# Optimization experiments

Hardware: AMD Instinct MI355X
Metric: run time of the kernel (lower is better)

## Reference

```python
import jax, jax.numpy as jnp
import numpy as np

N_NODES = 50000
N_EDGES = 600000
IN_FEATS = 128
N_HIDDEN = 128
N_CLASSES = 64


def setup_inputs() -> dict:
    key = jax.random.key(0)
    ks = jax.random.split(key, 10)
    x = jax.random.normal(ks[0], (N_NODES, IN_FEATS), dtype=jnp.float32)
    w = jax.random.uniform(ks[1], (N_EDGES,), dtype=jnp.float32)
    src = jax.random.randint(ks[2], (N_EDGES,), 0, N_NODES, dtype=jnp.int32)
    dst = jax.random.randint(ks[3], (N_EDGES,), 0, N_NODES, dtype=jnp.int32)
    W1 = jax.random.normal(ks[4], (IN_FEATS, N_HIDDEN), dtype=jnp.float32) * 0.05
    b1 = jnp.zeros((N_HIDDEN,), dtype=jnp.float32)
    W2 = jax.random.normal(ks[5], (N_HIDDEN, N_HIDDEN), dtype=jnp.float32) * 0.05
    b2 = jnp.zeros((N_HIDDEN,), dtype=jnp.float32)
    W3 = jax.random.normal(ks[6], (N_HIDDEN, N_CLASSES), dtype=jnp.float32) * 0.05
    b3 = jnp.zeros((N_CLASSES,), dtype=jnp.float32)
    return {"x": x, "w": w, "src": src, "dst": dst,
            "W1": W1, "b1": b1, "W2": W2, "b2": b2, "W3": W3, "b3": b3}


def _graph_conv(h, Wl, bl, w, src, dst, n_nodes):
    # dense linear transform
    h = h @ Wl + bl  # [N, d_out]
    # u_mul_e: gather source features, scale by edge weight
    m = h[src] * w[:, None]  # [E, d_out]
    # sum aggregation into destination nodes
    return jax.ops.segment_sum(m, dst, num_segments=n_nodes)  # [N, d_out]


def reference(x, w, src, dst, W1, b1, W2, b2, W3, b3):
    n = x.shape[0]
    h = jax.nn.relu(_graph_conv(x, W1, b1, w, src, dst, n))
    h = jax.nn.relu(_graph_conv(h, W2, b2, w, src, dst, n))
    return _graph_conv(h, W3, b3, w, src, dst, n)
```

## Files before the change

### kernel.cpp

```cpp
#include <hip/hip_runtime.h>


typedef __attribute__((ext_vector_type(8))) short short8;
typedef __attribute__((ext_vector_type(4))) float float4v;

constexpr int CAP  = 48;
constexpr int CPAD = 16;

__device__ inline unsigned bf16_rne(float f) {
    unsigned u = __float_as_uint(f);
    return (u + 0x7FFF + ((u >> 16) & 1)) >> 16;
}
__device__ inline float bf_lo(unsigned t) { return __uint_as_float(t << 16); }
__device__ inline float bf_hi(unsigned t) { return __uint_as_float(t & 0xFFFF0000u); }

__device__ inline void wprep_one(const float* __restrict__ Wm, int M, int tt,
                                 unsigned short* __restrict__ WfH,
                                 unsigned short* __restrict__ WfL) {
    const int FT = M / 16;
    int lane = tt & 63;
    int ft   = (tt >> 6) % FT;
    int ks   = tt / (64 * FT);
    int n     = ft * 16 + (lane & 15);
    int kbase = ks * 32 + (lane >> 4) * 8;
    #pragma unroll
    for (int j = 0; j < 8; j++) {
        float wv = Wm[(size_t)(kbase + j) * M + n];
        unsigned hb = bf16_rne(wv);
        float wh = __uint_as_float(hb << 16);
        unsigned lb = bf16_rne(wv - wh);
        WfH[(size_t)tt * 8 + j] = (unsigned short)hb;
        WfL[(size_t)tt * 8 + j] = (unsigned short)lb;
    }
}

__global__ void prep_kernel(const float* __restrict__ W1, const float* __restrict__ W2,
                            const float* __restrict__ W3,
                            unsigned short* WfH1, unsigned short* WfL1,
                            unsigned short* WfH2, unsigned short* WfL2,
                            unsigned short* WfH3, unsigned short* WfL3,
                            int* __restrict__ countsP, int N) {
    int t = blockIdx.x * blockDim.x + threadIdx.x;
    if (t < 2048)       wprep_one(W1, 128, t,        WfH1, WfL1);
    else if (t < 4096)  wprep_one(W2, 128, t - 2048, WfH2, WfL2);
    else if (t < 5120)  wprep_one(W3,  64, t - 4096, WfH3, WfL3);
    const int total = N * CPAD;
    for (int i = t; i < total; i += gridDim.x * blockDim.x) countsP[i] = 0;
}

__global__ void scatter_v5(const int* __restrict__ src, const int* __restrict__ dst,
                           const float* __restrict__ w, int* __restrict__ countsP,
                           int2* __restrict__ erec, int E) {
    int e = (blockIdx.x * blockDim.x + threadIdx.x) * 4;
    if (e + 3 < E) {
        int4   d4 = *(const int4*)(dst + e);
        int4   s4 = *(const int4*)(src + e);
        float4 w4 = *(const float4*)(w + e);
        int p0 = atomicAdd(&countsP[d4.x * CPAD], 1);
        int p1 = atomicAdd(&countsP[d4.y * CPAD], 1);
        int p2 = atomicAdd(&countsP[d4.z * CPAD], 1);
        int p3 = atomicAdd(&countsP[d4.w * CPAD], 1);
        if (p0 < CAP) erec[(size_t)d4.x * CAP + p0] = (int2){s4.x, __float_as_int(w4.x)};
        if (p1 < CAP) erec[(size_t)d4.y * CAP + p1] = (int2){s4.y, __float_as_int(w4.y)};
        if (p2 < CAP) erec[(size_t)d4.z * CAP + p2] = (int2){s4.z, __float_as_int(w4.z)};
        if (p3 < CAP) erec[(size_t)d4.w * CAP + p3] = (int2){s4.w, __float_as_int(w4.w)};
    } else {
        for (; e < E; e++) {
            int d = dst[e];
            int p = atomicAdd(&countsP[d * CPAD], 1);
            if (p < CAP) erec[(size_t)d * CAP + p] = (int2){src[e], __float_as_int(w[e])};
        }
    }
}

template <int M>
__global__ __launch_bounds__(256) void gemm_kernel(const float* __restrict__ H,
                                                   const unsigned short* __restrict__ WfH,
                                                   const unsigned short* __restrict__ WfL,
                                                   const float* __restrict__ bias,
                                                   unsigned short* __restrict__ T, int N) {
    const int K  = 128;
    const int KP = K + 4;
    const int FT = M / 16;
    __shared__ float Hs[64 * KP];

    const int node0 = blockIdx.x * 64;
    for (int i = threadIdx.x; i < 64 * (K / 4); i += 256) {
        int r = i / (K / 4), c = i % (K / 4);
        int node = node0 + r;
        float4 hv = {0, 0, 0, 0};
        if (node < N) hv = ((const float4*)(H + (size_t)node * K))[c];
        *(float4*)(Hs + r * KP + c * 4) = hv;
    }
    __syncthreads();

    const int wave = threadIdx.x >> 6;
    const int lane = threadIdx.x & 63;
    const int row  = lane & 15;
    const int ksub = (lane >> 4) * 8;
    const float* hrow = Hs + (wave * 16 + row) * KP;

    float4v acc[FT];
    #pragma unroll
    for (int ft = 0; ft < FT; ft++) acc[ft] = (float4v){0.f, 0.f, 0.f, 0.f};

    #pragma unroll
    for (int ks = 0; ks < 4; ks++) {
        const float* ap = hrow + ks * 32 + ksub;
        float4 a0 = *(const float4*)(ap);
        float4 a1 = *(const float4*)(ap + 4);
        float av[8] = {a0.x, a0.y, a0.z, a0.w, a1.x, a1.y, a1.z, a1.w};
        short8 ah, al;
        #pragma unroll
        for (int j = 0; j < 8; j++) {
            unsigned hb = bf16_rne(av[j]);
            float fh = __uint_as_float(hb << 16);
            ah[j] = (short)hb;
            al[j] = (short)bf16_rne(av[j] - fh);
        }
        #pragma unroll
        for (int ft = 0; ft < FT; ft++) {
            short8 bh = *(const short8*)(WfH + ((size_t)(ks * FT + ft) * 64 + lane) * 8);
            short8 bl = *(const short8*)(WfL + ((size_t)(ks * FT + ft) * 64 + lane) * 8);
            acc[ft] = __builtin_amdgcn_mfma_f32_16x16x32_bf16(ah, bh, acc[ft], 0, 0, 0);
            acc[ft] = __builtin_amdgcn_mfma_f32_16x16x32_bf16(al, bh, acc[ft], 0, 0, 0);
            acc[ft] = __builtin_amdgcn_mfma_f32_16x16x32_bf16(ah, bl, acc[ft], 0, 0, 0);
        }
    }

    const int col   = lane & 15;
    const int rbase = (lane >> 4) * 4;
    #pragma unroll
    for (int ft = 0; ft < FT; ft++) {
        int feat = ft * 16 + col;
        float bv = bias[feat];
        #pragma unroll
        for (int r = 0; r < 4; r++) {
            int node = node0 + wave * 16 + rbase + r;
            if (node < N)
                T[(size_t)node * M + feat] = (unsigned short)bf16_rne(acc[ft][r] + bv);
        }
    }
}

template <bool RELU>
__global__ void agg128_v4(const unsigned short* __restrict__ Tin,
                          const int* __restrict__ countsP,
                          const int2* __restrict__ erec,
                          float* __restrict__ OUT, int N) {
    const int wid  = threadIdx.x >> 6;
    const int lane = threadIdx.x & 63;
    const int v = blockIdx.x * 4 + wid;
    if (v >= N) return;
    const int c = min(countsP[v * CPAD], CAP);
    const int q  = lane >> 4;
    const int fo = (lane & 15) * 8;
    float a0 = 0, a1 = 0, a2 = 0, a3 = 0, a4 = 0, a5 = 0, a6 = 0, a7 = 0;
    if (c > 0) {
        const int2* eb = erec + (size_t)v * CAP;
        for (int i = 0; i < c; i += 16) {
            #pragma unroll
            for (int u = 0; u < 4; u++) {
                int idx = i + u * 4 + q;
                float wv = 0.f;
                int cl = idx < c ? idx : c - 1;
                int2 r = eb[cl];
                if (idx < c) wv = __int_as_float(r.y);
                uint4 t = *(const uint4*)(Tin + (size_t)r.x * 128 + fo);
                a0 = fmaf(wv, bf_lo(t.x), a0); a1 = fmaf(wv, bf_hi(t.x), a1);
                a2 = fmaf(wv, bf_lo(t.y), a2); a3 = fmaf(wv, bf_hi(t.y), a3);
                a4 = fmaf(wv, bf_lo(t.z), a4); a5 = fmaf(wv, bf_hi(t.z), a5);
                a6 = fmaf(wv, bf_lo(t.w), a6); a7 = fmaf(wv, bf_hi(t.w), a7);
            }
        }
        a0 += __shfl_xor(a0, 32); a1 += __shfl_xor(a1, 32);
        a2 += __shfl_xor(a2, 32); a3 += __shfl_xor(a3, 32);
        a4 += __shfl_xor(a4, 32); a5 += __shfl_xor(a5, 32);
        a6 += __shfl_xor(a6, 32); a7 += __shfl_xor(a7, 32);
        a0 += __shfl_xor(a0, 16); a1 += __shfl_xor(a1, 16);
        a2 += __shfl_xor(a2, 16); a3 += __shfl_xor(a3, 16);
        a4 += __shfl_xor(a4, 16); a5 += __shfl_xor(a5, 16);
        a6 += __shfl_xor(a6, 16); a7 += __shfl_xor(a7, 16);
    }
    if (lane < 16) {
        if (RELU) {
            a0 = fmaxf(a0, 0.f); a1 = fmaxf(a1, 0.f); a2 = fmaxf(a2, 0.f); a3 = fmaxf(a3, 0.f);
            a4 = fmaxf(a4, 0.f); a5 = fmaxf(a5, 0.f); a6 = fmaxf(a6, 0.f); a7 = fmaxf(a7, 0.f);
        }
        float4 o0 = {a0, a1, a2, a3};
        float4 o1 = {a4, a5, a6, a7};
        float* op = OUT + (size_t)v * 128 + fo;
        *(float4*)(op)     = o0;
        *(float4*)(op + 4) = o1;
    }
}

__global__ void agg_final_v4(const unsigned short* __restrict__ Tin,
                             const int* __restrict__ countsP,
                             const int2* __restrict__ erec,
                             float* __restrict__ OUT, int N) {
    const int wid  = threadIdx.x >> 6;
    const int lane = threadIdx.x & 63;
    const int v = blockIdx.x * 4 + wid;
    if (v >= N) return;
    const int c = min(countsP[v * CPAD], CAP);
    const int o8 = lane >> 3;
    const int fo = (lane & 7) * 8;
    float a0 = 0, a1 = 0, a2 = 0, a3 = 0, a4 = 0, a5 = 0, a6 = 0, a7 = 0;
    if (c > 0) {
        const int2* eb = erec + (size_t)v * CAP;
        for (int i = 0; i < c; i += 16) {
            #pragma unroll
            for (int u = 0; u < 2; u++) {
                int idx = i + u * 8 + o8;
                float wv = 0.f;
                int cl = idx < c ? idx : c - 1;
                int2 r = eb[cl];
                if (idx < c) wv = __int_as_float(r.y);
                uint4 t = *(const uint4*)(Tin + (size_t)r.x * 64 + fo);
                a0 = fmaf(wv, bf_lo(t.x), a0); a1 = fmaf(wv, bf_hi(t.x), a1);
                a2 = fmaf(wv, bf_lo(t.y), a2); a3 = fmaf(wv, bf_hi(t.y), a3);
                a4 = fmaf(wv, bf_lo(t.z), a4); a5 = fmaf(wv, bf_hi(t.z), a5);
                a6 = fmaf(wv, bf_lo(t.w), a6); a7 = fmaf(wv, bf_hi(t.w), a7);
            }
        }
        a0 += __shfl_xor(a0, 32); a1 += __shfl_xor(a1, 32);
        a2 += __shfl_xor(a2, 32); a3 += __shfl_xor(a3, 32);
        a4 += __shfl_xor(a4, 32); a5 += __shfl_xor(a5, 32);
        a6 += __shfl_xor(a6, 32); a7 += __shfl_xor(a7, 32);
        a0 += __shfl_xor(a0, 16); a1 += __shfl_xor(a1, 16);
        a2 += __shfl_xor(a2, 16); a3 += __shfl_xor(a3, 16);
        a4 += __shfl_xor(a4, 16); a5 += __shfl_xor(a5, 16);
        a6 += __shfl_xor(a6, 16); a7 += __shfl_xor(a7, 16);
        a0 += __shfl_xor(a0, 8);  a1 += __shfl_xor(a1, 8);
        a2 += __shfl_xor(a2, 8);  a3 += __shfl_xor(a3, 8);
        a4 += __shfl_xor(a4, 8);  a5 += __shfl_xor(a5, 8);
        a6 += __shfl_xor(a6, 8);  a7 += __shfl_xor(a7, 8);
    }
    if (lane < 8) {
        float4 o0 = {a0, a1, a2, a3};
        float4 o1 = {a4, a5, a6, a7};
        float* op = OUT + (size_t)v * 64 + fo;
        *(float4*)(op)     = o0;
        *(float4*)(op + 4) = o1;
    }
}

extern "C" void kernel_launch(void* const* d_in, const int* in_sizes, int n_in,
                              void* d_out, int out_size, void* d_ws, size_t ws_size,
                              hipStream_t stream) {
    const float* x   = (const float*)d_in[0];
    const float* w   = (const float*)d_in[1];
    const int*   src = (const int*)d_in[2];
    const int*   dst = (const int*)d_in[3];
    const float* W1  = (const float*)d_in[4];
    const float* b1  = (const float*)d_in[5];
    const float* W2  = (const float*)d_in[6];
    const float* b2  = (const float*)d_in[7];
    const float* W3  = (const float*)d_in[8];
    const float* b3  = (const float*)d_in[9];
    const int N = in_sizes[0] / 128;
    const int E = in_sizes[1];

    float* Hf            = (float*)d_ws;
    unsigned short* Tbf  = (unsigned short*)(Hf + (size_t)N * 128);
    int2* erec     = (int2*)(Tbf + (size_t)N * 128);
    int*  countsP  = (int*)(erec + (size_t)N * CAP);
    size_t off = (size_t)(countsP + (size_t)N * CPAD - (int*)d_ws);
    off = (off + 3) & ~(size_t)3;
    unsigned short* WfH1 = (unsigned short*)((int*)d_ws + off);
    unsigned short* WfL1 = WfH1 + 128 * 128;
    unsigned short* WfH2 = WfL1 + 128 * 128;
    unsigned short* WfL2 = WfH2 + 128 * 128;
    unsigned short* WfH3 = WfL2 + 128 * 128;
    unsigned short* WfL3 = WfH3 + 128 * 64;

    const int GB = (N + 63) / 64;
    const int AB = (N + 3) / 4;

    prep_kernel<<<96, 256, 0, stream>>>(W1, W2, W3, WfH1, WfL1, WfH2, WfL2,
                                        WfH3, WfL3, countsP, N);
    gemm_kernel<128><<<GB, 256, 0, stream>>>(x, WfH1, WfL1, b1, Tbf, N);
    scatter_v5<<<(E / 4 + 255) / 256, 256, 0, stream>>>(src, dst, w, countsP, erec, E);
    agg128_v4<true><<<AB, 256, 0, stream>>>(Tbf, countsP, erec, Hf, N);
    gemm_kernel<128><<<GB, 256, 0, stream>>>(Hf, WfH2, WfL2, b2, Tbf, N);
    agg128_v4<true><<<AB, 256, 0, stream>>>(Tbf, countsP, erec, Hf, N);
    gemm_kernel<64><<<GB, 256, 0, stream>>>(Hf, WfH3, WfL3, b3, Tbf, N);
    agg_final_v4<<<AB, 256, 0, stream>>>(Tbf, countsP, erec, (float*)d_out, N);
}
```

Baseline: 243.7 us.

## Fuse aggregation with following GEMM through shared memory

Replaces the aggregation kernel plus the separate dense GEMM with one kernel. Each 1024-thread block aggregates 16 nodes into shared memory, applies ReLU, then runs split-bf16 MFMA against the next layer's weights and writes bf16 output. This removes the fp32 hidden-feature round trip through global memory and two kernel launches. In exchange, large blocks must synchronise before the GEMM, and only FT of the 16 waves do GEMM work while the rest sit idle, which may lower occupancy.

```diff
diff --git a/kernel.cpp b/kernel.cpp
--- a/kernel.cpp
+++ b/kernel.cpp
@@ -143,55 +143,104 @@
     }
 }
 
-template <bool RELU>
-__global__ void agg128_v4(const unsigned short* __restrict__ Tin,
-                          const int* __restrict__ countsP,
-                          const int2* __restrict__ erec,
-                          float* __restrict__ OUT, int N) {
-    const int wid  = threadIdx.x >> 6;
+template <int MOUT>
+__global__ __launch_bounds__(1024) void fused_agg_gemm(
+    const unsigned short* __restrict__ Tin,
+    const int* __restrict__ countsP,
+    const int2* __restrict__ erec,
+    const unsigned short* __restrict__ WfH,
+    const unsigned short* __restrict__ WfL,
+    const float* __restrict__ bias,
+    unsigned short* __restrict__ Tout,
+    int N) {
+    const int KP = 132;
+    __shared__ float Hs[16 * KP];
+    const int wave = threadIdx.x >> 6;
     const int lane = threadIdx.x & 63;
-    const int v = blockIdx.x * 4 + wid;
-    if (v >= N) return;
-    const int c = min(countsP[v * CPAD], CAP);
-    const int q  = lane >> 4;
-    const int fo = (lane & 15) * 8;
-    float a0 = 0, a1 = 0, a2 = 0, a3 = 0, a4 = 0, a5 = 0, a6 = 0, a7 = 0;
-    if (c > 0) {
-        const int2* eb = erec + (size_t)v * CAP;
-        for (int i = 0; i < c; i += 16) {
-            #pragma unroll
-            for (int u = 0; u < 4; u++) {
-                int idx = i + u * 4 + q;
-                float wv = 0.f;
-                int cl = idx < c ? idx : c - 1;
-                int2 r = eb[cl];
-                if (idx < c) wv = __int_as_float(r.y);
-                uint4 t = *(const uint4*)(Tin + (size_t)r.x * 128 + fo);
-                a0 = fmaf(wv, bf_lo(t.x), a0); a1 = fmaf(wv, bf_hi(t.x), a1);
-                a2 = fmaf(wv, bf_lo(t.y), a2); a3 = fmaf(wv, bf_hi(t.y), a3);
-                a4 = fmaf(wv, bf_lo(t.z), a4); a5 = fmaf(wv, bf_hi(t.z), a5);
-                a6 = fmaf(wv, bf_lo(t.w), a6); a7 = fmaf(wv, bf_hi(t.w), a7);
+    const int v = blockIdx.x * 16 + wave;
+
+    {
+        const int q  = lane >> 4;
+        const int fo = (lane & 15) * 8;
+        float a0 = 0, a1 = 0, a2 = 0, a3 = 0, a4 = 0, a5 = 0, a6 = 0, a7 = 0;
+        if (v < N) {
+            const int c = min(countsP[v * CPAD], CAP);
+            if (c > 0) {
+                const int2* eb = erec + (size_t)v * CAP;
+                for (int i = 0; i < c; i += 16) {
+                    #pragma unroll
+                    for (int u = 0; u < 4; u++) {
+                        int idx = i + u * 4 + q;
+                        float wv = 0.f;
+                        int cl = idx < c ? idx : c - 1;
+                        int2 r = eb[cl];
+                        if (idx < c) wv = __int_as_float(r.y);
+                        uint4 t = *(const uint4*)(Tin + (size_t)r.x * 128 + fo);
+                        a0 = fmaf(wv, bf_lo(t.x), a0); a1 = fmaf(wv, bf_hi(t.x), a1);
+                        a2 = fmaf(wv, bf_lo(t.y), a2); a3 = fmaf(wv, bf_hi(t.y), a3);
+                        a4 = fmaf(wv, bf_lo(t.z), a4); a5 = fmaf(wv, bf_hi(t.z), a5);
+                        a6 = fmaf(wv, bf_lo(t.w), a6); a7 = fmaf(wv, bf_hi(t.w), a7);
+                    }
+                }
+                a0 += __shfl_xor(a0, 32); a1 += __shfl_xor(a1, 32);
+                a2 += __shfl_xor(a2, 32); a3 += __shfl_xor(a3, 32);
+                a4 += __shfl_xor(a4, 32); a5 += __shfl_xor(a5, 32);
+                a6 += __shfl_xor(a6, 32); a7 += __shfl_xor(a7, 32);
+                a0 += __shfl_xor(a0, 16); a1 += __shfl_xor(a1, 16);
+                a2 += __shfl_xor(a2, 16); a3 += __shfl_xor(a3, 16);
+                a4 += __shfl_xor(a4, 16); a5 += __shfl_xor(a5, 16);
+                a6 += __shfl_xor(a6, 16); a7 += __shfl_xor(a7, 16);
             }
         }
-        a0 += __shfl_xor(a0, 32); a1 += __shfl_xor(a1, 32);
-        a2 += __shfl_xor(a2, 32); a3 += __shfl_xor(a3, 32);
-        a4 += __shfl_xor(a4, 32); a5 += __shfl_xor(a5, 32);
-        a6 += __shfl_xor(a6, 32); a7 += __shfl_xor(a7, 32);
-        a0 += __shfl_xor(a0, 16); a1 += __shfl_xor(a1, 16);
-        a2 += __shfl_xor(a2, 16); a3 += __shfl_xor(a3, 16);
-        a4 += __shfl_xor(a4, 16); a5 += __shfl_xor(a5, 16);
-        a6 += __shfl_xor(a6, 16); a7 += __shfl_xor(a7, 16);
-    }
-    if (lane < 16) {
-        if (RELU) {
+        if (lane < 16) {
             a0 = fmaxf(a0, 0.f); a1 = fmaxf(a1, 0.f); a2 = fmaxf(a2, 0.f); a3 = fmaxf(a3, 0.f);
             a4 = fmaxf(a4, 0.f); a5 = fmaxf(a5, 0.f); a6 = fmaxf(a6, 0.f); a7 = fmaxf(a7, 0.f);
-        }
-        float4 o0 = {a0, a1, a2, a3};
-        float4 o1 = {a4, a5, a6, a7};
-        float* op = OUT + (size_t)v * 128 + fo;
-        *(float4*)(op)     = o0;
-        *(float4*)(op + 4) = o1;
+            float* hp = Hs + wave * KP + lane * 8;
+            float4 o0 = {a0, a1, a2, a3};
+            float4 o1 = {a4, a5, a6, a7};
+            *(float4*)(hp)     = o0;
+            *(float4*)(hp + 4) = o1;
+        }
+    }
+    __syncthreads();
+
+    const int FT = MOUT / 16;
+    if (wave < FT) {
+        const int ft   = wave;
+        const int row  = lane & 15;
+        const int ksub = (lane >> 4) * 8;
+        const float* hrow = Hs + row * KP;
+        float4v acc = (float4v){0.f, 0.f, 0.f, 0.f};
+        #pragma unroll
+        for (int ks = 0; ks < 4; ks++) {
+            const float* ap = hrow + ks * 32 + ksub;
+            float4 A0 = *(const float4*)(ap);
+            float4 A1 = *(const float4*)(ap + 4);
+            float av[8] = {A0.x, A0.y, A0.z, A0.w, A1.x, A1.y, A1.z, A1.w};
+            short8 ah, al;
+            #pragma unroll
+            for (int j = 0; j < 8; j++) {
+                unsigned hb = bf16_rne(av[j]);
+                float fh = __uint_as_float(hb << 16);
+                ah[j] = (short)hb;
+                al[j] = (short)bf16_rne(av[j] - fh);
+            }
+            short8 bh = *(const short8*)(WfH + ((size_t)(ks * FT + ft) * 64 + lane) * 8);
+            short8 bl = *(const short8*)(WfL + ((size_t)(ks * FT + ft) * 64 + lane) * 8);
+            acc = __builtin_amdgcn_mfma_f32_16x16x32_bf16(ah, bh, acc, 0, 0, 0);
+            acc = __builtin_amdgcn_mfma_f32_16x16x32_bf16(al, bh, acc, 0, 0, 0);
+            acc = __builtin_amdgcn_mfma_f32_16x16x32_bf16(ah, bl, acc, 0, 0, 0);
+        }
+        const int col   = lane & 15;
+        const int rbase = (lane >> 4) * 4;
+        int feat = ft * 16 + col;
+        float bv = bias[feat];
+        #pragma unroll
+        for (int r = 0; r < 4; r++) {
+            int node = blockIdx.x * 16 + rbase + r;
+            if (node < N)
+                Tout[(size_t)node * MOUT + feat] = (unsigned short)bf16_rne(acc[r] + bv);
+        }
     }
 }
 
@@ -262,9 +311,9 @@
     const int N = in_sizes[0] / 128;
     const int E = in_sizes[1];
 
-    float* Hf            = (float*)d_ws;
-    unsigned short* Tbf  = (unsigned short*)(Hf + (size_t)N * 128);
-    int2* erec     = (int2*)(Tbf + (size_t)N * 128);
+    unsigned short* TbfA = (unsigned short*)d_ws;
+    unsigned short* TbfB = TbfA + (size_t)N * 128;
+    int2* erec     = (int2*)(TbfB + (size_t)N * 128);
     int*  countsP  = (int*)(erec + (size_t)N * CAP);
     size_t off = (size_t)(countsP + (size_t)N * CPAD - (int*)d_ws);
     off = (off + 3) & ~(size_t)3;
@@ -276,15 +325,16 @@
     unsigned short* WfL3 = WfH3 + 128 * 64;
 
     const int GB = (N + 63) / 64;
+    const int FB = (N + 15) / 16;
     const int AB = (N + 3) / 4;
 
     prep_kernel<<<96, 256, 0, stream>>>(W1, W2, W3, WfH1, WfL1, WfH2, WfL2,
                                         WfH3, WfL3, countsP, N);
-    gemm_kernel<128><<<GB, 256, 0, stream>>>(x, WfH1, WfL1, b1, Tbf, N);
+    gemm_kernel<128><<<GB, 256, 0, stream>>>(x, WfH1, WfL1, b1, TbfA, N);
     scatter_v5<<<(E / 4 + 255) / 256, 256, 0, stream>>>(src, dst, w, countsP, erec, E);
-    agg128_v4<true><<<AB, 256, 0, stream>>>(Tbf, countsP, erec, Hf, N);
-    gemm_kernel<128><<<GB, 256, 0, stream>>>(Hf, WfH2, WfL2, b2, Tbf, N);
-    agg128_v4<true><<<AB, 256, 0, stream>>>(Tbf, countsP, erec, Hf, N);
-    gemm_kernel<64><<<GB, 256, 0, stream>>>(Hf, WfH3, WfL3, b3, Tbf, N);
-    agg_final_v4<<<AB, 256, 0, stream>>>(Tbf, countsP, erec, (float*)d_out, N);
-}
+    fused_agg_gemm<128><<<FB, 1024, 0, stream>>>(TbfA, countsP, erec,
+                                                 WfH2, WfL2, b2, TbfB, N);
+    fused_agg_gemm<64><<<FB, 1024, 0, stream>>>(TbfB, countsP, erec,
+                                                WfH3, WfL3, b3, TbfA, N);
+    agg_final_v4<<<AB, 256, 0, stream>>>(TbfA, countsP, erec, (float*)d_out, N);
+}
```

Measured after the change: 241.1 us. Within noise of the previous version (-1.1%).
